# Optimization experiments

Measured on AMD Instinct MI355X. Metric: run time of the kernel, lower is better.

## Reference

```python
import jax, jax.numpy as jnp
from jax import lax
import numpy as np

B, L, D = 2048, 100, 64      # batch, max_len, embedding_dim
K = 64                       # embedding_num (codebook entries)
CB = K * 8                   # code_book_dim = 512 (== D*8 encoder out channels)
ITEMS = 1_000_000
EPS = 1e-3                   # tf.layers.batch_normalization default epsilon


def setup_inputs() -> dict:
    key = jax.random.key(0)
    ks = jax.random.split(key, 16)
    w = lambda i, shape: jax.random.normal(ks[i], shape, dtype=jnp.float32) * 0.05
    z = lambda c: jnp.zeros((c,), jnp.float32)
    o = lambda c: jnp.ones((c,), jnp.float32)
    return {
        "history_item_ids": jax.random.randint(ks[0], (B, L), 0, ITEMS, dtype=jnp.int32),
        "history_item_masks": jax.random.randint(ks[1], (B, L), 0, 2, dtype=jnp.int32),
        "item_embedding_table": jax.random.normal(ks[2], (ITEMS, D), dtype=jnp.float32),
        "user_book": jax.random.normal(ks[3], (K, CB), dtype=jnp.float32),
        "e_w1": w(4, (2, 2, D, 2 * D)), "e_b1": z(2 * D), "e_g1": o(2 * D), "e_be1": z(2 * D),
        "e_w2": w(5, (2, 2, 2 * D, 4 * D)), "e_b2": z(4 * D), "e_g2": o(4 * D), "e_be2": z(4 * D),
        "e_w3": w(6, (2, 2, 4 * D, 8 * D)), "e_b3": z(8 * D),
        "d_w1": w(7, (2, 2, 8 * D, 4 * D)), "d_b1": z(4 * D), "d_g1": o(4 * D), "d_be1": z(4 * D),
        "d_w2": w(8, (2, 2, 4 * D, 2 * D)), "d_b2": z(2 * D), "d_g2": o(2 * D), "d_be2": z(2 * D),
        "d_w3": w(9, (2, 2, 2 * D, D)), "d_b3": z(D),
    }


def _forward(history_item_ids, history_item_masks, item_embedding_table, user_book,
             e_w1, e_b1, e_g1, e_be1, e_w2, e_b2, e_g2, e_be2, e_w3, e_b3,
             d_w1, d_b1, d_g1, d_be1, d_w2, d_b2, d_g2, d_be2, d_w3, d_b3):
    dn = ('NHWC', 'HWIO', 'NHWC')
    bn = lambda x, g, b: x * (g / jnp.sqrt(1.0 + EPS)) + b  # inference BN: moving mean 0, var 1
    conv = lambda x, w_, b_: lax.conv_general_dilated(x, w_, (1, 1), 'VALID', dimension_numbers=dn) + b_
    deconv = lambda x, w_, b_: lax.conv_transpose(x, w_, (1, 1), 'VALID', dimension_numbers=dn) + b_

    mask = (history_item_masks >= 1).astype(jnp.float32)               # [B,L]
    hist = item_embedding_table[history_item_ids] * mask[..., None]    # [B,L,D]

    H = int(L ** 0.5); W = L // H
    h = hist.reshape(-1, H, W, D)
    h = jax.nn.relu(bn(conv(h, e_w1, e_b1), e_g1, e_be1))              # [B,9,9,2D]
    h = jax.nn.relu(bn(conv(h, e_w2, e_b2), e_g2, e_be2))              # [B,8,8,4D]
    x_encode = conv(h, e_w3, e_b3)                                     # [B,7,7,CB]

    # nearest-neighbor codebook lookup (get_quantized)
    flat = x_encode.reshape(-1, CB)                                    # [B*49,CB]
    dist = ((flat * flat).sum(1, keepdims=True)
            + (user_book * user_book).sum(1)
            - 2.0 * flat @ user_book.T)                                # [B*49,K]
    idx = jnp.argmin(dist, axis=1)
    quantized = user_book[idx].reshape(x_encode.shape)                 # [B,7,7,CB]

    # straight-through estimator
    st = x_encode + lax.stop_gradient(quantized - x_encode)
    g = jax.nn.relu(bn(deconv(st, d_w1, d_b1), d_g1, d_be1))           # [B,8,8,4D]
    g = jax.nn.relu(bn(deconv(g, d_w2, d_b2), d_g2, d_be2))            # [B,9,9,2D]
    vq_x = deconv(g, d_w3, d_b3).reshape(hist.shape)                   # [B,L,D]

    vq_mean = vq_x.sum(1) / mask.sum(-1, keepdims=True)                # [B,D]
    mse = lambda a, b: jnp.mean((a - b) ** 2)
    beta = 0.25
    vqvae_loss = (mse(hist, vq_x)
                  + mse(quantized, lax.stop_gradient(x_encode))
                  + beta * mse(x_encode, lax.stop_gradient(quantized)))
    return vq_mean, vq_x, vqvae_loss


def reference(history_item_ids, history_item_masks, item_embedding_table, user_book,
              e_w1, e_b1, e_g1, e_be1, e_w2, e_b2, e_g2, e_be2, e_w3, e_b3,
              d_w1, d_b1, d_g1, d_be1, d_w2, d_b2, d_g2, d_be2, d_w3, d_b3):
    return _forward(history_item_ids, history_item_masks, item_embedding_table, user_book,
                    e_w1, e_b1, e_g1, e_be1, e_w2, e_b2, e_g2, e_be2, e_w3, e_b3,
                    d_w1, d_b1, d_g1, d_be1, d_w2, d_b2, d_g2, d_be2, d_w3, d_b3)
```

## Files before the change

### kernel.cpp

```cpp
#include <hip/hip_runtime.h>
#include <hip/hip_bf16.h>
#include <cstdint>
#include <cstddef>


typedef __attribute__((ext_vector_type(8))) short short8v;
typedef __attribute__((ext_vector_type(4))) float f32x4;

constexpr int B  = 2048;
constexpr int L  = 100;
constexpr int K  = 64;
constexpr int CB = 512;
#define MARGIN 0.1f

constexpr size_t R0_OFF  = 0;
constexpr size_t R1_OFF  = 51380224;
constexpr size_t IDX_OFF = 84934656;
constexpr size_t CBN_OFF = 85035008;
constexpr size_t CNT_OFF = 85035072;
constexpr size_t ACC_OFF = 85035088;
constexpr size_t WL_OFF  = 85035104;
constexpr size_t WB_OFF  = 85135456;

constexpr size_t EW1H=0,       EW1L=32768;
constexpr size_t EW2H=65536,   EW2L=196608;
constexpr size_t EW3H=327680;
constexpr size_t DW2H=851968,  DW3H=983040;
constexpr size_t W3BH=1015808, W3BL=1081344;

constexpr size_t BW1_OFF  = WB_OFF + 573440;
constexpr size_t DOTB_OFF = BW1_OFF + 65536;

__device__ inline ushort bf16_hi(float f){ __hip_bfloat16 h=__float2bfloat16(f); return *(ushort*)&h; }
__device__ inline float  bf16_tof(ushort u){ __hip_bfloat16 h; *(ushort*)&h=u; return __bfloat162float(h); }

__device__ void wtrans(const float* __restrict__ w, int IC, int OC,
                       ushort* __restrict__ hi, ushort* __restrict__ lo,
                       int gid, int gsz)
{
    int tot = 4*IC*OC;
    for (int i = gid; i < tot; i += gsz) {
        int kk = i/(IC*OC), r = i - kk*(IC*OC), ic = r/OC, oc = r - ic*OC;
        float v = w[i];
        ushort h = bf16_hi(v);
        size_t dst = ((size_t)kk*OC + oc)*IC + ic;
        hi[dst] = h;
        if (lo) lo[dst] = bf16_hi(v - bf16_tof(h));
    }
}

__global__ __launch_bounds__(256)
void wprep_k(const float* e1, const float* e2, const float* e3,
             const float* d2, const float* d3, ushort* wb)
{
    int gid = blockIdx.x*256 + threadIdx.x, gsz = gridDim.x*256;
    wtrans(e1,  64, 128, wb+EW1H, wb+EW1L, gid, gsz);
    wtrans(e2, 128, 256, wb+EW2H, wb+EW2L, gid, gsz);
    wtrans(e3, 256, 512, wb+EW3H, nullptr, gid, gsz);
    wtrans(d2, 256, 128, wb+DW2H, nullptr, gid, gsz);
    wtrans(d3, 128,  64, wb+DW3H, nullptr, gid, gsz);
}

__global__ __launch_bounds__(256)
void w3b_k(const float* __restrict__ e_w3, const float* __restrict__ book,
           ushort* __restrict__ wb)
{
    const int kk = blockIdx.x >> 6, k = blockIdx.x & 63, ic = threadIdx.x;
    const float4* wr = (const float4*)(e_w3 + ((size_t)(kk*256)+ic)*512);
    const float4* br = (const float4*)(book + (size_t)k*512);
    float s = 0.f;
    for (int c = 0; c < 128; ++c) {
        float4 a = wr[c], bb = br[c];
        s = fmaf(a.x,bb.x,fmaf(a.y,bb.y,fmaf(a.z,bb.z,fmaf(a.w,bb.w,s))));
    }
    size_t dst = ((size_t)(kk*64+k))*256 + ic;
    ushort h = bf16_hi(s);
    wb[W3BH+dst] = h;
    wb[W3BL+dst] = bf16_hi(s - bf16_tof(h));
}

__global__ __launch_bounds__(256)
void bw1_k(const float* __restrict__ d_w1, const float* __restrict__ book,
           float* __restrict__ bw1)
{
    const int tap = blockIdx.x >> 6, k = blockIdx.x & 63, oc = threadIdx.x;
    const float* br = book + (size_t)k*512;
    const float* wr = d_w1 + (size_t)(tap*512)*256 + oc;
    float s = 0.f;
    for (int ic = 0; ic < 512; ++ic)
        s = fmaf(br[ic], wr[(size_t)ic*256], s);
    bw1[((size_t)(tap*64+k))*256 + oc] = s;
}

__global__ __launch_bounds__(256)
void prep_k(const float* __restrict__ book, const float* __restrict__ e_b3,
            float* __restrict__ cbn, float* __restrict__ dotb,
            float* __restrict__ acc, int* __restrict__ cnt)
{
    const int t = threadIdx.x;
    if (t < 64) {
        const float* r = book + t * 512;
        float s = 0.f, d = 0.f;
        for (int c = 0; c < 512; ++c) { s = fmaf(r[c], r[c], s); d = fmaf(e_b3[c], r[c], d); }
        cbn[t] = s; dotb[t] = d;
    }
    if (t == 64 || t == 65) acc[t-64] = 0.f;
    if (t == 66) *cnt = 0;
}

template<int IH,int IW,int IC,int OC,int PAD,int MODE,bool HASBN,bool SPLIT,
         int OCS,int ICC,int MT,int OUTFMT,bool FUSE,int SMP,bool DBUF>
__global__ __launch_bounds__(256)
void sconv_k(const uint* __restrict__ in_pk, const ushort* __restrict__ in_bf,
             const int* __restrict__ ids, const int* __restrict__ masks,
             const float* __restrict__ table,
             const ushort* __restrict__ wt_hi, const ushort* __restrict__ wt_lo,
             const float* __restrict__ bias, const float* __restrict__ gamma,
             const float* __restrict__ beta,
             float* __restrict__ out_f, uint* __restrict__ out_pk,
             ushort* __restrict__ out_bf, float* __restrict__ out_mean,
             float* __restrict__ acc_g)
{
    constexpr int OH=IH+2*PAD-1, OW=IW+2*PAD-1, NPOS=OH*OW, IHW=IH*IW;
    constexpr int OCB=OC/OCS, NPW=OCB/4, NT=NPW/16;
    constexpr int NCH=IC/ICC, KS=ICC/32;
    constexpr int PL=SPLIT?2:1;
    constexpr int NB=(DBUF && NCH>1)?2:1;
    constexpr int AROWS=IHW+1, RB=ICC*2;
    constexpr int C8=ICC/8;
    constexpr int NITEMS=SMP*IHW*C8;
    constexpr int SI=(NITEMS+255)/256;
    constexpr bool EXACT=(SI*256==NITEMS);
    constexpr int SPLB=AROWS*RB;
    constexpr int SAMB=PL*SPLB;
    constexpr int BUFB=SMP*SAMB;

    __shared__ ushort s_a[NB*SMP*PL*AROWS*ICC];
    char* sb=(char*)s_a;

    const int v=blockIdx.x, r8=v&7, iv=v>>3;
    const int b0 = (r8*(B/SMP/8) + iv/OCS)*SMP;
    const int sl = iv - (iv/OCS)*OCS;

    const int tid=threadIdx.x, lane=tid&63, wv=tid>>6;
    const int l15=lane&15, lq=lane>>4;
    const int n0=sl*OCB + wv*NPW;

    int arow[4][MT];
    #pragma unroll
    for(int kk=0;kk<4;++kk){
        const int ky=kk>>1, kx=kk&1;
        #pragma unroll
        for(int m=0;m<MT;++m){
            int p=m*16+l15;
            int py=p/OW, px=p-py*OW;
            int ty=py+ky-PAD, tx=px+kx-PAD;
            bool ok=(p<NPOS)&&((unsigned)ty<(unsigned)IH)&&((unsigned)tx<(unsigned)IW);
            arow[kk][m]= ok ? ty*IW+tx : IHW;
        }
    }

    f32x4 acc[SMP][MT][NT];
    #pragma unroll
    for(int s=0;s<SMP;++s)
        #pragma unroll
        for(int m=0;m<MT;++m)
            #pragma unroll
            for(int n=0;n<NT;++n) acc[s][m][n]=(f32x4)0.0f;

    uint4 r0[SI];
    uint4 r1[(MODE==1||MODE==3)?SI:1];
    float msk[(MODE==1)?SI:1];

    auto stage_load=[&](int c){
        const int ic0=c*ICC;
        #pragma unroll
        for(int t=0;t<SI;++t){
            int idx=tid+t*256;
            if(EXACT || idx<NITEMS){
                int row=idx/C8, g=idx-row*C8;
                int s=row/IHW, r=row-s*IHW;
                if constexpr(MODE==1){
                    int id=ids[(b0+s)*L+r];
                    msk[t]=(masks[(b0+s)*L+r]>=1)?1.f:0.f;
                    const float* src=table+(size_t)id*64+g*8;
                    r0[t]=*(const uint4*)src;
                    r1[t]=*(const uint4*)(src+4);
                } else if constexpr(MODE==3){
                    const uint* src=in_pk+((size_t)(b0+s)*IHW+r)*IC+ic0+g*8;
                    r0[t]=*(const uint4*)src;
                    r1[t]=*(const uint4*)(src+4);
                } else {
                    r0[t]=*(const uint4*)(in_bf+((size_t)(b0+s)*IHW+r)*IC+ic0+g*8);
                }
            }
        }
    };

    auto stage_write=[&](int bufb){
        #pragma unroll
        for(int t=0;t<SI;++t){
            int idx=tid+t*256;
            if(EXACT || idx<NITEMS){
                int row=idx/C8, g=idx-row*C8;
                int s=row/IHW, r=row-s*IHW;
                int boff=bufb + s*SAMB + r*RB + ((g^(r&7))<<4);
                if constexpr(MODE==1){
                    const float* f0=(const float*)&r0[t];
                    const float* f1=(const float*)&r1[t];
                    float vv[8]={f0[0]*msk[t],f0[1]*msk[t],f0[2]*msk[t],f0[3]*msk[t],
                                 f1[0]*msk[t],f1[1]*msk[t],f1[2]*msk[t],f1[3]*msk[t]};
                    ushort hh[8], ll[8];
                    #pragma unroll
                    for(int j=0;j<8;++j){ hh[j]=bf16_hi(vv[j]); ll[j]=bf16_hi(vv[j]-bf16_tof(hh[j])); }
                    *(uint4*)(sb+boff)=*(uint4*)hh;
                    *(uint4*)(sb+SPLB+boff)=*(uint4*)ll;
                } else if constexpr(MODE==3){
                    const uint* u0=(const uint*)&r0[t];
                    const uint* u1=(const uint*)&r1[t];
                    ushort hh[8], ll[8];
                    #pragma unroll
                    for(int j=0;j<4;++j){ hh[j]=(ushort)(u0[j]&0xffffu); ll[j]=(ushort)(u0[j]>>16); }
                    #pragma unroll
                    for(int j=0;j<4;++j){ hh[4+j]=(ushort)(u1[j]&0xffffu); ll[4+j]=(ushort)(u1[j]>>16); }
                    *(uint4*)(sb+boff)=*(uint4*)hh;
                    *(uint4*)(sb+SPLB+boff)=*(uint4*)ll;
                } else {
                    *(uint4*)(sb+boff)=r0[t];
                }
            }
        }
    };

    auto zero_rows=[&](){
        for(int z=tid; z<NB*SMP*PL*C8; z+=256){
            int nb=z/(SMP*PL*C8), rz=z-nb*(SMP*PL*C8);
            int s=rz/(PL*C8), rz2=rz-s*(PL*C8), pl=rz2/C8, g=rz2-pl*C8;
            *(uint4*)(sb + nb*BUFB + s*SAMB + pl*SPLB + IHW*RB + (g<<4)) = make_uint4(0,0,0,0);
        }
    };

    auto do_mfma=[&](int bufb, int c){
        const int ic0=c*ICC;
        __builtin_amdgcn_s_setprio(1);
        #pragma unroll
        for(int kk=0;kk<4;++kk){
            #pragma unroll
            for(int ks=0;ks<KS;++ks){
                short8v bhv[NT]; short8v blv[SPLIT?NT:1];
                #pragma unroll
                for(int n=0;n<NT;++n){
                    int col=n0+n*16+l15;
                    size_t widx=((size_t)kk*OC+col)*IC+ic0+ks*32+lq*8;
                    bhv[n]=*(const short8v*)(wt_hi+widx);
                    if constexpr(SPLIT) blv[n]=*(const short8v*)(wt_lo+widx);
                }
                #pragma unroll
                for(int s=0;s<SMP;++s){
                    const int sbase=bufb + s*SAMB;
                    #pragma unroll
                    for(int m=0;m<MT;++m){
                        int off=sbase + arow[kk][m]*RB + ((((ks<<2)|lq)^(arow[kk][m]&7))<<4);
                        short8v ah=*(const short8v*)(sb+off);
                        if constexpr(SPLIT){
                            short8v al=*(const short8v*)(sb+SPLB+off);
                            #pragma unroll
                            for(int n=0;n<NT;++n){
                                acc[s][m][n]=__builtin_amdgcn_mfma_f32_16x16x32_bf16(ah,bhv[n],acc[s][m][n],0,0,0);
                                acc[s][m][n]=__builtin_amdgcn_mfma_f32_16x16x32_bf16(ah,blv[n],acc[s][m][n],0,0,0);
                                acc[s][m][n]=__builtin_amdgcn_mfma_f32_16x16x32_bf16(al,bhv[n],acc[s][m][n],0,0,0);
                            }
                        } else {
                            #pragma unroll
                            for(int n=0;n<NT;++n)
                                acc[s][m][n]=__builtin_amdgcn_mfma_f32_16x16x32_bf16(ah,bhv[n],acc[s][m][n],0,0,0);
                        }
                    }
                }
            }
        }
        __builtin_amdgcn_s_setprio(0);
    };

    if constexpr(NB==1){
        stage_load(0);
        zero_rows();
        for(int c=0;c<NCH;++c){
            if(c) __syncthreads();
            stage_write(0);
            __syncthreads();
            if(c+1<NCH) stage_load(c+1);
            do_mfma(0,c);
        }
    } else {
        stage_load(0);
        stage_write(0);
        zero_rows();
        __syncthreads();
        for(int c=0;c<NCH;++c){
            if(c+1<NCH) stage_load(c+1);
            do_mfma((c&1)*BUFB,c);
            if(c+1<NCH){
                stage_write(((c+1)&1)*BUFB);
                __syncthreads();
            }
        }
    }

    const float rs=(float)(1.0/sqrt(1.0+1e-3));
    float lsum=0.f, colsum=0.f;
    #pragma unroll
    for(int s=0;s<SMP;++s){
        const int b=b0+s;
        #pragma unroll
        for(int n=0;n<NT;++n){
            int col=n0+n*16+l15;
            float bi=bias[col];
            float gsc=0.f, bt=0.f;
            if constexpr(HASBN){ gsc=gamma[col]*rs; bt=beta[col]; }
            #pragma unroll
            for(int m=0;m<MT;++m){
                #pragma unroll
                for(int j=0;j<4;++j){
                    int p=m*16+lq*4+j;
                    if(p<NPOS){
                        float vx=acc[s][m][n][j]+bi;
                        if constexpr(HASBN) vx=fmaxf(fmaf(vx,gsc,bt),0.f);
                        size_t g=(size_t)b*NPOS+p;
                        if constexpr(OUTFMT==0){
                            out_f[g*OC+col]=vx;
                        } else if constexpr(OUTFMT==1){
                            ushort h=bf16_hi(vx);
                            ushort lo=bf16_hi(vx-bf16_tof(h));
                            out_pk[g*OC+col]=(uint)h | ((uint)lo<<16);
                        } else {
                            out_bf[g*OC+col]=bf16_hi(vx);
                        }
                        if constexpr(FUSE){
                            int id=ids[b*L+p];
                            float mm=(masks[b*L+p]>=1)?1.f:0.f;
                            float h=table[(size_t)id*64+col]*mm;
                            float df=h-vx;
                            lsum=fmaf(df,df,lsum);
                            colsum+=vx;
                        }
                    }
                }
            }
        }
    }

    if constexpr(FUSE){
        const int b=b0;
        float mc=0.f;
        for(int l=lane;l<L;l+=64) mc += (masks[b*L+l]>=1)?1.f:0.f;
        #pragma unroll
        for(int off=32;off;off>>=1) mc+=__shfl_xor(mc,off);
        colsum += __shfl_xor(colsum,16);
        colsum += __shfl_xor(colsum,32);
        if(lq==0) out_mean[b*64 + n0 + l15] = colsum/mc;
        #pragma unroll
        for(int off=32;off;off>>=1) lsum+=__shfl_xor(lsum,off);
        __syncthreads();
        float* red=(float*)sb;
        if(lane==0) red[wv]=lsum;
        __syncthreads();
        if(tid==0) atomicAdd(acc_g+0, red[0]+red[1]+red[2]+red[3]);
    }
}

__device__ inline int xswz(int row, int sl){ return (sl ^ (row&31) ^ ((row>>3)&7)) << 4; }

__global__ __launch_bounds__(512)
void xsq_k(const uint* __restrict__ in_pk,
           const ushort* __restrict__ wx,
           const float* __restrict__ xbias,
           float* __restrict__ acc_g)
{
    constexpr int NPOS=49, OW=7, MT=4;
    constexpr int ROWB=512;

    __shared__ ushort s_a[64*256];
    char* sb=(char*)s_a;

    const int v=blockIdx.x;
    const int b=(v&7)*(B/8)+(v>>3);
    const int tid=threadIdx.x, lane=tid&63, wv=tid>>6;
    const int l15=lane&15, lq=lane>>4;

    #pragma unroll
    for(int t=0;t<4;++t){
        int idx=tid+t*512;
        int row=idx>>5, sl=idx&31;
        const uint* src=in_pk+((size_t)b*64+row)*256+sl*8;
        uint4 u0=*(const uint4*)src, u1=*(const uint4*)(src+4);
        const uint* p0=(const uint*)&u0;
        const uint* p1=(const uint*)&u1;
        ushort hh[8];
        #pragma unroll
        for(int j=0;j<4;++j){ hh[j]=(ushort)(p0[j]&0xffffu); hh[4+j]=(ushort)(p1[j]&0xffffu); }
        *(uint4*)(sb+row*ROWB+xswz(row,sl))=*(uint4*)hh;
    }
    __syncthreads();

    int arow[4][MT];
    #pragma unroll
    for(int kk=0;kk<4;++kk){
        const int ky=kk>>1, kx=kk&1;
        #pragma unroll
        for(int m=0;m<MT;++m){
            int p=m*16+l15;
            int py=p/OW, px=p-py*OW;
            arow[kk][m]= (p<NPOS) ? (py+ky)*8+(px+kx) : 0;
        }
    }

    float xs=0.f;
    #pragma unroll
    for(int cc=0;cc<2;++cc){
        f32x4 accx[MT][2];
        #pragma unroll
        for(int m=0;m<MT;++m){ accx[m][0]=(f32x4)0.0f; accx[m][1]=(f32x4)0.0f; }
        const int col0=wv*64+cc*32+l15;
        __builtin_amdgcn_s_setprio(1);
        #pragma unroll
        for(int kk=0;kk<4;++kk){
            #pragma unroll
            for(int ks=0;ks<8;++ks){
                short8v bx0=*(const short8v*)(wx+((size_t)kk*512+col0)*256+ks*32+lq*8);
                short8v bx1=*(const short8v*)(wx+((size_t)kk*512+col0+16)*256+ks*32+lq*8);
                const int slb=ks*4+lq;
                #pragma unroll
                for(int m=0;m<MT;++m){
                    int r=arow[kk][m];
                    short8v ah=*(const short8v*)(sb+r*ROWB+xswz(r,slb));
                    accx[m][0]=__builtin_amdgcn_mfma_f32_16x16x32_bf16(ah,bx0,accx[m][0],0,0,0);
                    accx[m][1]=__builtin_amdgcn_mfma_f32_16x16x32_bf16(ah,bx1,accx[m][1],0,0,0);
                }
            }
        }
        __builtin_amdgcn_s_setprio(0);
        #pragma unroll
        for(int n=0;n<2;++n){
            const float bi=xbias[col0+n*16];
            #pragma unroll
            for(int m=0;m<MT;++m){
                #pragma unroll
                for(int j=0;j<4;++j){
                    int p=m*16+lq*4+j;
                    if(p<NPOS){ float vv=accx[m][n][j]+bi; xs=fmaf(vv,vv,xs); }
                }
            }
        }
    }
    #pragma unroll
    for(int off=32;off;off>>=1) xs+=__shfl_xor(xs,off);

    __syncthreads();
    float* f=(float*)sb;
    if(lane==0) f[wv]=xs;
    __syncthreads();
    if(tid==0) atomicAdd(acc_g+1, f[0]+f[1]+f[2]+f[3]+f[4]+f[5]+f[6]+f[7]);
}

__global__ __launch_bounds__(512)
void dot_k(const uint* __restrict__ in_pk,
           const ushort* __restrict__ w3bh, const ushort* __restrict__ w3bl,
           const float* __restrict__ cbn, const float* __restrict__ dotb,
           int* __restrict__ qidx, float* __restrict__ acc_g,
           int* __restrict__ cnt, int* __restrict__ wl)
{
    constexpr int NPOS=49, OW=7, MT=4;
    constexpr int ROWB=512;
    constexpr int PLB=64*ROWB;

    __shared__ ushort s_a[2*64*256];
    char* sb=(char*)s_a;

    const int v=blockIdx.x;
    const int b=(v&7)*(B/8)+(v>>3);
    const int tid=threadIdx.x, lane=tid&63, wv=tid>>6;
    const int l15=lane&15, lq=lane>>4;

    #pragma unroll
    for(int t=0;t<4;++t){
        int idx=tid+t*512;
        int row=idx>>5, sl=idx&31;
        const uint* src=in_pk+((size_t)b*64+row)*256+sl*8;
        uint4 u0=*(const uint4*)src, u1=*(const uint4*)(src+4);
        const uint* p0=(const uint*)&u0;
        const uint* p1=(const uint*)&u1;
        ushort hh[8], ll[8];
        #pragma unroll
        for(int j=0;j<4;++j){ hh[j]=(ushort)(p0[j]&0xffffu); ll[j]=(ushort)(p0[j]>>16); }
        #pragma unroll
        for(int j=0;j<4;++j){ hh[4+j]=(ushort)(p1[j]&0xffffu); ll[4+j]=(ushort)(p1[j]>>16); }
        int boff=row*ROWB+xswz(row,sl);
        *(uint4*)(sb+boff)=*(uint4*)hh;
        *(uint4*)(sb+PLB+boff)=*(uint4*)ll;
    }
    __syncthreads();

    int arow[4][MT];
    #pragma unroll
    for(int kk=0;kk<4;++kk){
        const int ky=kk>>1, kx=kk&1;
        #pragma unroll
        for(int m=0;m<MT;++m){
            int p=m*16+l15;
            int py=p/OW, px=p-py*OW;
            arow[kk][m]= (p<NPOS) ? (py+ky)*8+(px+kx) : 0;
        }
    }

    const int cold=(wv&3)*16+l15;
    const int ks0=(wv>>2)*4;
    f32x4 accd[MT];
    #pragma unroll
    for(int m=0;m<MT;++m) accd[m]=(f32x4)0.0f;

    __builtin_amdgcn_s_setprio(1);
    #pragma unroll
    for(int kk=0;kk<4;++kk){
        #pragma unroll
        for(int kq2=0;kq2<4;++kq2){
            const int ks=ks0+kq2;
            size_t wdx=((size_t)kk*64+cold)*256+ks*32+lq*8;
            short8v bdh=*(const short8v*)(w3bh+wdx);
            short8v bdl=*(const short8v*)(w3bl+wdx);
            const int slb=ks*4+lq;
            #pragma unroll
            for(int m=0;m<MT;++m){
                int r=arow[kk][m];
                int off=r*ROWB+xswz(r,slb);
                short8v ah=*(const short8v*)(sb+off);
                short8v al=*(const short8v*)(sb+PLB+off);
                accd[m]=__builtin_amdgcn_mfma_f32_16x16x32_bf16(ah,bdh,accd[m],0,0,0);
                accd[m]=__builtin_amdgcn_mfma_f32_16x16x32_bf16(ah,bdl,accd[m],0,0,0);
                accd[m]=__builtin_amdgcn_mfma_f32_16x16x32_bf16(al,bdh,accd[m],0,0,0);
            }
        }
    }
    __builtin_amdgcn_s_setprio(0);

    __syncthreads();
    float* f=(float*)sb;
    if(wv>=4){
        float* dst=f+((wv-4)*64+lane)*16;
        #pragma unroll
        for(int m=0;m<MT;++m){
            #pragma unroll
            for(int j=0;j<4;++j) dst[m*4+j]=accd[m][j];
        }
    }
    __syncthreads();

    float* sd1=f+4096;
    int*   sk =(int*)(f+4096+256);
    float* sd2=f+4096+512;
    if(wv<4){
        const float* srcp=f+(wv*64+lane)*16;
        float cb=cbn[cold], db=dotb[cold];
        #pragma unroll
        for(int m=0;m<MT;++m){
            #pragma unroll
            for(int j=0;j<4;++j){
                int p=m*16+lq*4+j;
                float dtot=accd[m][j]+srcp[m*4+j];
                float d1=cb-2.f*(dtot+db);
                int   k1=cold;
                float d2=3.4e38f;
                #pragma unroll
                for(int off=1;off<16;off<<=1){
                    float od1=__shfl_xor(d1,off);
                    int   ok1=__shfl_xor(k1,off);
                    float od2=__shfl_xor(d2,off);
                    if(od1<d1 || (od1==d1 && ok1<k1)){ d2=fminf(d1,od2); d1=od1; k1=ok1; }
                    else                              { d2=fminf(d2,od1); }
                }
                if(l15==0 && p<NPOS){ sd1[p*4+wv]=d1; sk[p*4+wv]=k1; sd2[p*4+wv]=d2; }
            }
        }
    }
    __syncthreads();

    {
        float lsum=0.f;
        if(tid<NPOS){
            float d1=sd1[tid*4+0]; int k1=sk[tid*4+0]; float d2=sd2[tid*4+0];
            #pragma unroll
            for(int w=1;w<4;++w){
                float D1=sd1[tid*4+w]; int K1=sk[tid*4+w]; float D2=sd2[tid*4+w];
                if(D1<d1){ d2=fminf(d1,D2); d1=D1; k1=K1; }
                else     { d2=fminf(d2,D1); }
            }
            qidx[b*49+tid]=k1;
            if(d2-d1<=MARGIN){ int t=atomicAdd(cnt,1); wl[t]=b*49+tid; }
            lsum=d1;
        }
        if(tid<64){
            #pragma unroll
            for(int off=32;off;off>>=1) lsum+=__shfl_xor(lsum,off);
            if(tid==0) atomicAdd(acc_g+1, lsum);
        }
    }
}

__global__ __launch_bounds__(256)
void dgather_k(const int* __restrict__ qidx, const float* __restrict__ bw1,
               const float* __restrict__ b1, const float* __restrict__ g1s,
               const float* __restrict__ be1, ushort* __restrict__ G1)
{
    const int b=blockIdx.x, tid=threadIdx.x;
    const int pg=tid>>2, og=(tid&3)*64;
    const int py=pg>>3, px=pg&7;

    float a[64];
    #pragma unroll
    for(int j=0;j<64;++j) a[j]=0.f;

    #pragma unroll
    for(int tap=0;tap<4;++tap){
        int iy=py+(tap>>1)-1, ix=px+(tap&1)-1;
        if((unsigned)iy<7u && (unsigned)ix<7u){
            int kq=qidx[b*49+iy*7+ix];
            const float4* src=(const float4*)(bw1+((size_t)(tap*64+kq))*256+og);
            #pragma unroll
            for(int j=0;j<16;++j){
                float4 vv=src[j];
                a[4*j+0]+=vv.x; a[4*j+1]+=vv.y; a[4*j+2]+=vv.z; a[4*j+3]+=vv.w;
            }
        }
    }
    const float rs=(float)(1.0/sqrt(1.0+1e-3));
    #pragma unroll
    for(int j=0;j<64;++j){
        int col=og+j;
        float vv=a[j]+b1[col];
        vv=fmaxf(fmaf(vv, g1s[col]*rs, be1[col]), 0.f);
        G1[((size_t)b*64+pg)*256+col]=bf16_hi(vv);
    }
}

__global__ __launch_bounds__(256)
void recompute_k(const int* __restrict__ wl, const int* __restrict__ cnt,
                 const int* __restrict__ ids, const int* __restrict__ masks,
                 const float* __restrict__ table, const float* __restrict__ book,
                 const float* __restrict__ e_w1, const float* __restrict__ e_b1,
                 const float* __restrict__ e_g1, const float* __restrict__ e_be1,
                 const float* __restrict__ e_w2, const float* __restrict__ e_b2,
                 const float* __restrict__ e_g2, const float* __restrict__ e_be2,
                 const float* __restrict__ e_w3, const float* __restrict__ e_b3,
                 int* __restrict__ qidx)
{
    __shared__ double s_h[16*64];
    __shared__ double s_a1[9*128];
    __shared__ double s_a2[4*256];
    __shared__ double s_x[512];
    __shared__ double s_d[256];

    const int tid = threadIdx.x;
    const double rs = 1.0 / sqrt(1.0 + 1e-3);
    const int n = *cnt;

    for (int wi = blockIdx.x; wi < n; wi += gridDim.x) {
        const int row = wl[wi];
        const int b = row / 49, p = row % 49;
        const int py = p / 7, px = p % 7;

        for (int i = tid; i < 16*64; i += 256) {
            int cell = i >> 6, d = i & 63;
            int l = (py + (cell >> 2)) * 10 + (px + (cell & 3));
            int id = ids[b*100 + l];
            double m = (masks[b*100 + l] >= 1) ? 1.0 : 0.0;
            s_h[i] = (double)table[(size_t)id*64 + d] * m;
        }
        __syncthreads();

        for (int i = tid; i < 9*128; i += 256) {
            int cell = i >> 7, oc = i & 127;
            int ry = cell / 3, rx = cell % 3;
            double s = 0.0;
            #pragma unroll
            for (int kk = 0; kk < 4; ++kk) {
                int icell = (ry + (kk>>1))*4 + (rx + (kk&1));
                const double* hh = s_h + icell*64;
                const float* ww = e_w1 + (kk*64)*128 + oc;
                for (int ic = 0; ic < 64; ++ic)
                    s = fma(hh[ic], (double)ww[ic*128], s);
            }
            s += (double)e_b1[oc];
            s = s * ((double)e_g1[oc] * rs) + (double)e_be1[oc];
            s_a1[i] = s > 0.0 ? s : 0.0;
        }
        __syncthreads();

        for (int i = tid; i < 4*256; i += 256) {
            int cell = i >> 8, oc = i & 255;
            int qy = cell >> 1, qx = cell & 1;
            double s = 0.0;
            #pragma unroll
            for (int kk = 0; kk < 4; ++kk) {
                int icell = (qy + (kk>>1))*3 + (qx + (kk&1));
                const double* aa = s_a1 + icell*128;
                const float* ww = e_w2 + (kk*128)*256 + oc;
                for (int ic = 0; ic < 128; ++ic)
                    s = fma(aa[ic], (double)ww[ic*256], s);
            }
            s += (double)e_b2[oc];
            s = s * ((double)e_g2[oc] * rs) + (double)e_be2[oc];
            s_a2[i] = s > 0.0 ? s : 0.0;
        }
        __syncthreads();

        for (int i = tid; i < 512; i += 256) {
            double s = 0.0;
            #pragma unroll
            for (int kk = 0; kk < 4; ++kk) {
                const double* aa = s_a2 + kk*256;
                const float* ww = e_w3 + (kk*256)*512 + i;
                for (int ic = 0; ic < 256; ++ic)
                    s = fma(aa[ic], (double)ww[ic*512], s);
            }
            s_x[i] = s + (double)e_b3[i];
        }
        __syncthreads();

        {
            int k = tid & 63, seg = tid >> 6;
            const float* cr = book + k*512 + seg*128;
            const double* xr = s_x + seg*128;
            double s = 0.0;
            for (int c = 0; c < 128; ++c) {
                double dd = xr[c] - (double)cr[c];
                s = fma(dd, dd, s);
            }
            s_d[seg*64 + k] = s;
        }
        __syncthreads();

        if (tid < 64) {
            double dv = s_d[tid] + s_d[64+tid] + s_d[128+tid] + s_d[192+tid];
            int kk2 = tid;
            #pragma unroll
            for (int off = 32; off > 0; off >>= 1) {
                double od = __shfl_xor(dv, off);
                int    ok = __shfl_xor(kk2, off);
                if (od < dv || (od == dv && ok < kk2)) { dv = od; kk2 = ok; }
            }
            if (tid == 0) qidx[row] = kk2;
        }
        __syncthreads();
    }
}

__global__ void loss_k(const float* __restrict__ acc, float* __restrict__ out_loss)
{
    float l1 = acc[0] / 13107200.f;
    float l2 = acc[1] / 51380224.f;
    out_loss[0] = l1 + l2 + 0.25f * l2;
}

extern "C" void kernel_launch(void* const* d_in, const int* in_sizes, int n_in,
                              void* d_out, int out_size, void* d_ws, size_t ws_size,
                              hipStream_t stream)
{
    const int*   ids   = (const int*)d_in[0];
    const int*   masks = (const int*)d_in[1];
    const float* table = (const float*)d_in[2];
    const float* book  = (const float*)d_in[3];
    const float* e_w1  = (const float*)d_in[4];
    const float* e_b1  = (const float*)d_in[5];
    const float* e_g1  = (const float*)d_in[6];
    const float* e_be1 = (const float*)d_in[7];
    const float* e_w2  = (const float*)d_in[8];
    const float* e_b2  = (const float*)d_in[9];
    const float* e_g2  = (const float*)d_in[10];
    const float* e_be2 = (const float*)d_in[11];
    const float* e_w3  = (const float*)d_in[12];
    const float* e_b3  = (const float*)d_in[13];
    const float* d_w1  = (const float*)d_in[14];
    const float* d_b1  = (const float*)d_in[15];
    const float* d_g1  = (const float*)d_in[16];
    const float* d_be1 = (const float*)d_in[17];
    const float* d_w2  = (const float*)d_in[18];
    const float* d_b2  = (const float*)d_in[19];
    const float* d_g2  = (const float*)d_in[20];
    const float* d_be2 = (const float*)d_in[21];
    const float* d_w3  = (const float*)d_in[22];
    const float* d_b3  = (const float*)d_in[23];

    float*  ws  = (float*)d_ws;
    uint*   A1P = (uint*)(ws + R0_OFF);
    uint*   A2P = (uint*)(ws + R1_OFF);
    ushort* G1  = (ushort*)(ws + R1_OFF);
    ushort* G2  = (ushort*)(ws + R0_OFF);
    int*    IDX = (int*)(ws + IDX_OFF);
    float*  CBN = ws + CBN_OFF;
    int*    CNT = (int*)(ws + CNT_OFF);
    float*  ACC = ws + ACC_OFF;
    int*    WL  = (int*)(ws + WL_OFF);
    ushort* WB  = (ushort*)(ws + WB_OFF);
    float*  BW1 = ws + BW1_OFF;
    float*  DOTB= ws + DOTB_OFF;

    float* out_mean = (float*)d_out;
    float* out_vqx  = (float*)d_out + (size_t)B * 64;
    float* out_loss = (float*)d_out + (size_t)B * 64 + (size_t)B * L * 64;

    prep_k<<<1, 256, 0, stream>>>(book, e_b3, CBN, DOTB, ACC, CNT);
    wprep_k<<<512, 256, 0, stream>>>(e_w1, e_w2, e_w3, d_w2, d_w3, WB);
    w3b_k<<<256, 256, 0, stream>>>(e_w3, book, WB);
    bw1_k<<<256, 256, 0, stream>>>(d_w1, book, BW1);

    sconv_k<10,10, 64,128,0,1,true ,true ,1, 64,6,1,false,1,true ><<<B,   256,0,stream>>>(
        nullptr, nullptr, ids, masks, table,
        WB+EW1H, WB+EW1L, e_b1, e_g1, e_be1, nullptr, A1P, nullptr, nullptr, nullptr);
    sconv_k< 9, 9,128,256,0,3,true ,true ,2, 64,4,1,false,1,true ><<<B*2, 256,0,stream>>>(
        A1P, nullptr, nullptr, nullptr, nullptr,
        WB+EW2H, WB+EW2L, e_b2, e_g2, e_be2, nullptr, A2P, nullptr, nullptr, nullptr);

    xsq_k<<<B, 512, 0, stream>>>(A2P, WB+EW3H, e_b3, ACC);
    dot_k<<<B, 512, 0, stream>>>(A2P, WB+W3BH, WB+W3BL, CBN, DOTB, IDX, ACC, CNT, WL);

    recompute_k<<<512, 256, 0, stream>>>(WL, CNT, ids, masks, table, book,
                                         e_w1, e_b1, e_g1, e_be1,
                                         e_w2, e_b2, e_g2, e_be2,
                                         e_w3, e_b3, IDX);

    dgather_k<<<B, 256, 0, stream>>>(IDX, BW1, d_b1, d_g1, d_be1, G1);
    sconv_k< 8, 8,256,128,1,4,true ,false,1, 64,6,2,false,1,true ><<<B,   256,0,stream>>>(
        nullptr, G1, nullptr, nullptr, nullptr,
        WB+DW2H, nullptr, d_b2, d_g2, d_be2, nullptr, nullptr, G2, nullptr, nullptr);
    sconv_k< 9, 9,128, 64,1,4,false,false,1, 64,7,0,true ,1,true ><<<B,   256,0,stream>>>(
        nullptr, G2, ids, masks, table,
        WB+DW3H, nullptr, d_b3, nullptr, nullptr, out_vqx, nullptr, nullptr, out_mean, ACC);

    loss_k<<<1, 1, 0, stream>>>(ACC, out_loss);
}
```

Before: 1.149 ms.

## Process worklist rows in pairs in fp64 recompute kernel to share weight loads

The fp64 recompute kernel now handles two worklist rows per iteration, so each weight element loaded from global memory feeds two accumulations instead of one. The inner loops also split into two independent accumulators to shorten the FMA dependency chain, and the grid grows from 512 to 1024 blocks. This is meant to halve weight traffic per row and raise instruction-level parallelism. In exchange it doubles shared memory per block, which can cut occupancy, and the larger grid mostly idles if the worklist is short.

After: 2.369 ms. +106.2%, slower.

```diff
diff --git a/kernel.cpp b/kernel.cpp
--- a/kernel.cpp
+++ b/kernel.cpp
@@ -653,102 +653,134 @@
                  const float* __restrict__ e_w3, const float* __restrict__ e_b3,
                  int* __restrict__ qidx)
 {
-    __shared__ double s_h[16*64];
-    __shared__ double s_a1[9*128];
-    __shared__ double s_a2[4*256];
-    __shared__ double s_x[512];
-    __shared__ double s_d[256];
+    __shared__ double s_h[2][16*64];
+    __shared__ double s_a1[2][9*128];
+    __shared__ double s_a2[2][4*256];
+    __shared__ double s_x[2][512];
+    __shared__ double s_d[2][256];
 
     const int tid = threadIdx.x;
     const double rs = 1.0 / sqrt(1.0 + 1e-3);
     const int n = *cnt;
-
-    for (int wi = blockIdx.x; wi < n; wi += gridDim.x) {
-        const int row = wl[wi];
-        const int b = row / 49, p = row % 49;
-        const int py = p / 7, px = p % 7;
+    const int npairs = (n + 1) >> 1;
+
+    for (int pi = blockIdx.x; pi < npairs; pi += gridDim.x) {
+        const int rowA = wl[2*pi];
+        const int rowB = (2*pi+1 < n) ? wl[2*pi+1] : rowA;
+        const int bb[2] = { rowA/49, rowB/49 };
+        const int pp[2] = { rowA%49, rowB%49 };
 
         for (int i = tid; i < 16*64; i += 256) {
             int cell = i >> 6, d = i & 63;
-            int l = (py + (cell >> 2)) * 10 + (px + (cell & 3));
-            int id = ids[b*100 + l];
-            double m = (masks[b*100 + l] >= 1) ? 1.0 : 0.0;
-            s_h[i] = (double)table[(size_t)id*64 + d] * m;
+            #pragma unroll
+            for (int r2 = 0; r2 < 2; ++r2) {
+                int py = pp[r2]/7, px = pp[r2]%7;
+                int l = (py + (cell >> 2)) * 10 + (px + (cell & 3));
+                int id = ids[bb[r2]*100 + l];
+                double m = (masks[bb[r2]*100 + l] >= 1) ? 1.0 : 0.0;
+                s_h[r2][i] = (double)table[(size_t)id*64 + d] * m;
+            }
         }
         __syncthreads();
 
         for (int i = tid; i < 9*128; i += 256) {
             int cell = i >> 7, oc = i & 127;
             int ry = cell / 3, rx = cell % 3;
-            double s = 0.0;
+            double sA0=0,sA1=0,sB0=0,sB1=0;
             #pragma unroll
             for (int kk = 0; kk < 4; ++kk) {
                 int icell = (ry + (kk>>1))*4 + (rx + (kk&1));
-                const double* hh = s_h + icell*64;
+                const double* h0 = s_h[0] + icell*64;
+                const double* h1 = s_h[1] + icell*64;
                 const float* ww = e_w1 + (kk*64)*128 + oc;
-                for (int ic = 0; ic < 64; ++ic)
-                    s = fma(hh[ic], (double)ww[ic*128], s);
-            }
-            s += (double)e_b1[oc];
-            s = s * ((double)e_g1[oc] * rs) + (double)e_be1[oc];
-            s_a1[i] = s > 0.0 ? s : 0.0;
+                for (int ic = 0; ic < 64; ic += 2) {
+                    double w0 = (double)ww[ic*128], w1 = (double)ww[(ic+1)*128];
+                    sA0 = fma(h0[ic],   w0, sA0);
+                    sA1 = fma(h0[ic+1], w1, sA1);
+                    sB0 = fma(h1[ic],   w0, sB0);
+                    sB1 = fma(h1[ic+1], w1, sB1);
+                }
+            }
+            double g1 = (double)e_g1[oc]*rs, be1v=(double)e_be1[oc], b1v=(double)e_b1[oc];
+            double sA = (sA0+sA1) + b1v; sA = sA*g1 + be1v; s_a1[0][i] = sA>0.0?sA:0.0;
+            double sB = (sB0+sB1) + b1v; sB = sB*g1 + be1v; s_a1[1][i] = sB>0.0?sB:0.0;
         }
         __syncthreads();
 
         for (int i = tid; i < 4*256; i += 256) {
             int cell = i >> 8, oc = i & 255;
             int qy = cell >> 1, qx = cell & 1;
-            double s = 0.0;
+            double sA0=0,sA1=0,sB0=0,sB1=0;
             #pragma unroll
             for (int kk = 0; kk < 4; ++kk) {
                 int icell = (qy + (kk>>1))*3 + (qx + (kk&1));
-                const double* aa = s_a1 + icell*128;
+                const double* a0 = s_a1[0] + icell*128;
+                const double* a1 = s_a1[1] + icell*128;
                 const float* ww = e_w2 + (kk*128)*256 + oc;
-                for (int ic = 0; ic < 128; ++ic)
-                    s = fma(aa[ic], (double)ww[ic*256], s);
-            }
-            s += (double)e_b2[oc];
-            s = s * ((double)e_g2[oc] * rs) + (double)e_be2[oc];
-            s_a2[i] = s > 0.0 ? s : 0.0;
+                for (int ic = 0; ic < 128; ic += 2) {
+                    double w0 = (double)ww[ic*256], w1 = (double)ww[(ic+1)*256];
+                    sA0 = fma(a0[ic],   w0, sA0);
+                    sA1 = fma(a0[ic+1], w1, sA1);
+                    sB0 = fma(a1[ic],   w0, sB0);
+                    sB1 = fma(a1[ic+1], w1, sB1);
+                }
+            }
+            double g2 = (double)e_g2[oc]*rs, be2v=(double)e_be2[oc], b2v=(double)e_b2[oc];
+            double sA = (sA0+sA1) + b2v; sA = sA*g2 + be2v; s_a2[0][i] = sA>0.0?sA:0.0;
+            double sB = (sB0+sB1) + b2v; sB = sB*g2 + be2v; s_a2[1][i] = sB>0.0?sB:0.0;
         }
         __syncthreads();
 
         for (int i = tid; i < 512; i += 256) {
-            double s = 0.0;
+            double sA0=0,sA1=0,sB0=0,sB1=0;
             #pragma unroll
             for (int kk = 0; kk < 4; ++kk) {
-                const double* aa = s_a2 + kk*256;
+                const double* a0 = s_a2[0] + kk*256;
+                const double* a1 = s_a2[1] + kk*256;
                 const float* ww = e_w3 + (kk*256)*512 + i;
-                for (int ic = 0; ic < 256; ++ic)
-                    s = fma(aa[ic], (double)ww[ic*512], s);
-            }
-            s_x[i] = s + (double)e_b3[i];
+                for (int ic = 0; ic < 256; ic += 2) {
+                    double w0 = (double)ww[(size_t)ic*512], w1 = (double)ww[(size_t)(ic+1)*512];
+                    sA0 = fma(a0[ic],   w0, sA0);
+                    sA1 = fma(a0[ic+1], w1, sA1);
+                    sB0 = fma(a1[ic],   w0, sB0);
+                    sB1 = fma(a1[ic+1], w1, sB1);
+                }
+            }
+            double b3v = (double)e_b3[i];
+            s_x[0][i] = (sA0+sA1) + b3v;
+            s_x[1][i] = (sB0+sB1) + b3v;
         }
         __syncthreads();
 
         {
             int k = tid & 63, seg = tid >> 6;
-            const float* cr = book + k*512 + seg*128;
-            const double* xr = s_x + seg*128;
-            double s = 0.0;
-            for (int c = 0; c < 128; ++c) {
-                double dd = xr[c] - (double)cr[c];
-                s = fma(dd, dd, s);
-            }
-            s_d[seg*64 + k] = s;
+            #pragma unroll
+            for (int r2 = 0; r2 < 2; ++r2) {
+                const float* cr = book + k*512 + seg*128;
+                const double* xr = s_x[r2] + seg*128;
+                double s0 = 0.0, s1 = 0.0;
+                for (int c = 0; c < 128; c += 2) {
+                    double d0 = xr[c]   - (double)cr[c];
+                    double d1 = xr[c+1] - (double)cr[c+1];
+                    s0 = fma(d0, d0, s0);
+                    s1 = fma(d1, d1, s1);
+                }
+                s_d[r2][seg*64 + k] = s0 + s1;
+            }
         }
         __syncthreads();
 
-        if (tid < 64) {
-            double dv = s_d[tid] + s_d[64+tid] + s_d[128+tid] + s_d[192+tid];
-            int kk2 = tid;
+        if (tid < 128) {
+            int r2 = tid >> 6, lane2 = tid & 63;
+            double dv = s_d[r2][lane2] + s_d[r2][64+lane2] + s_d[r2][128+lane2] + s_d[r2][192+lane2];
+            int kk2 = lane2;
             #pragma unroll
             for (int off = 32; off > 0; off >>= 1) {
                 double od = __shfl_xor(dv, off);
                 int    ok = __shfl_xor(kk2, off);
                 if (od < dv || (od == dv && ok < kk2)) { dv = od; kk2 = ok; }
             }
-            if (tid == 0) qidx[row] = kk2;
+            if (lane2 == 0) qidx[r2 ? rowB : rowA] = kk2;
         }
         __syncthreads();
     }
@@ -823,10 +855,10 @@
     xsq_k<<<B, 512, 0, stream>>>(A2P, WB+EW3H, e_b3, ACC);
     dot_k<<<B, 512, 0, stream>>>(A2P, WB+W3BH, WB+W3BL, CBN, DOTB, IDX, ACC, CNT, WL);
 
-    recompute_k<<<512, 256, 0, stream>>>(WL, CNT, ids, masks, table, book,
-                                         e_w1, e_b1, e_g1, e_be1,
-                                         e_w2, e_b2, e_g2, e_be2,
-                                         e_w3, e_b3, IDX);
+    recompute_k<<<1024, 256, 0, stream>>>(WL, CNT, ids, masks, table, book,
+                                          e_w1, e_b1, e_g1, e_be1,
+                                          e_w2, e_b2, e_g2, e_be2,
+                                          e_w3, e_b3, IDX);
 
     dgather_k<<<B, 256, 0, stream>>>(IDX, BW1, d_b1, d_g1, d_be1, G1);
     sconv_k< 8, 8,256,128,1,4,true ,false,1, 64,6,2,false,1,true ><<<B,   256,0,stream>>>(
```
